# Optimization experiments

Hardware: AMD Instinct MI355X
Metric: run time of the kernel (lower is better)

## Reference

```python
import jax, jax.numpy as jnp
import numpy as np

B, N, DIM = 2, 2048, 2048
N_HEAD, N_KV_HEAD = 32, 8
HEAD_DIM = DIM // N_HEAD  # 64
NEG_INF = -1e9


def setup_inputs() -> dict:
    key = jax.random.key(0)
    ks = jax.random.split(key, 4)
    x = jax.random.normal(ks[0], (B, N, DIM), dtype=jnp.float32)
    Wq = jax.random.normal(ks[1], (DIM, N_HEAD * HEAD_DIM), dtype=jnp.float32) * (DIM ** -0.5)
    Wkv = jax.random.normal(ks[2], (DIM, 2 * N_KV_HEAD * HEAD_DIM), dtype=jnp.float32) * (DIM ** -0.5)
    Wo = jax.random.normal(ks[3], (N_HEAD * HEAD_DIM, DIM), dtype=jnp.float32) * (DIM ** -0.5)
    # RoPE angles: freqs = 1/theta^(2i/d), angle[p, i] = p * freqs[i]
    freqs = 1.0 / (10000.0 ** (jnp.arange(0, HEAD_DIM, 2, dtype=jnp.float32) / HEAD_DIM))
    angles = jnp.arange(N, dtype=jnp.float32)[:, None] * freqs[None, :]  # (N, HEAD_DIM//2)
    rope_cos = jnp.cos(angles)
    rope_sin = jnp.sin(angles)
    # additive causal mask (n, n)
    mask = jnp.where(jnp.tril(jnp.ones((N, N), dtype=bool)), 0.0, NEG_INF).astype(jnp.float32)
    return {"x": x, "Wq": Wq, "Wkv": Wkv, "Wo": Wo, "rope_cos": rope_cos, "rope_sin": rope_sin, "mask": mask, "start_pos": 0}


def apply_rope(x, cos, sin):
    # x: (b, n, h, d); cos/sin: (n, d//2). Complex mult on interleaved pairs.
    xr = x.reshape(*x.shape[:-1], HEAD_DIM // 2, 2)
    xe, xo = xr[..., 0], xr[..., 1]
    c = cos[None, :, None, :]
    s = sin[None, :, None, :]
    yr = xe * c - xo * s
    yi = xe * s + xo * c
    return jnp.stack([yr, yi], axis=-1).reshape(x.shape)


def reference(x, Wq, Wkv, Wo, rope_cos, rope_sin, mask, start_pos):
    b, n, _ = x.shape
    q = (x @ Wq).reshape(b, n, N_HEAD, HEAD_DIM)
    kv = (x @ Wkv).reshape(b, n, 2, N_KV_HEAD, HEAD_DIM)
    k, v = kv[:, :, 0], kv[:, :, 1]
    q = apply_rope(q, rope_cos, rope_sin)
    k = apply_rope(k, rope_cos, rope_sin)
    # repeat kv heads: 'b n h d -> b n (r h) d'
    r = N_HEAD // N_KV_HEAD
    k = jnp.tile(k, (1, 1, r, 1))
    v = jnp.tile(v, (1, 1, r, 1))
    scale = HEAD_DIM ** -0.5
    attn = jnp.einsum('bnhd,bmhd->bhnm', q, k) * scale + mask[None, None]
    attn = jax.nn.softmax(attn, axis=-1)
    out = jnp.einsum('bhnm,bmhd->bnhd', attn, v).reshape(b, n, N_HEAD * HEAD_DIM)
    return out @ Wo
```

## Files before the change

kernel.cpp:

```cpp
#include <hip/hip_runtime.h>


#define BSZ  2
#define NSEQ 2048
#define DIMD 2048
#define NH   32
#define NKV  8
#define HD   64
#define TK   32

typedef __bf16 bf16x8 __attribute__((ext_vector_type(8)));
typedef __bf16 bf16x4 __attribute__((ext_vector_type(4)));
typedef __bf16 bf16x2 __attribute__((ext_vector_type(2)));
typedef float  floatx4 __attribute__((ext_vector_type(4)));
typedef float  floatx16 __attribute__((ext_vector_type(16)));
typedef unsigned int uintx4 __attribute__((ext_vector_type(4)));

#define MFMA16(a, b, c) __builtin_amdgcn_mfma_f32_16x16x32_bf16(a, b, c, 0, 0, 0)
#define MFMA32(a, b, c) __builtin_amdgcn_mfma_f32_32x32x16_bf16(a, b, c, 0, 0, 0)

#define WAITV(n) asm volatile("s_waitcnt vmcnt(" #n ")" ::: "memory")

__device__ __forceinline__ void barrier_nodrain() {
    asm volatile("" ::: "memory");
    __builtin_amdgcn_sched_barrier(0);
    __builtin_amdgcn_s_barrier();
    __builtin_amdgcn_sched_barrier(0);
    asm volatile("" ::: "memory");
}

__device__ __forceinline__ void gload_lds16(const void* g, void* l) {
    __builtin_amdgcn_global_load_lds((const __attribute__((address_space(1))) void*)g,
                                     (__attribute__((address_space(3))) void*)l, 16, 0, 0);
}

__device__ __forceinline__ unsigned pk2(float a, float b) {
    bf16x2 t; t[0] = (__bf16)a; t[1] = (__bf16)b;
    return __builtin_bit_cast(unsigned, t);
}

__global__ void cvt_x_kernel(const float* __restrict__ in, __bf16* __restrict__ out, int n4) {
    int i = blockIdx.x * blockDim.x + threadIdx.x;
    if (i >= n4) return;
    float4 v = ((const float4*)in)[i];
    bf16x4 o;
    o[0] = (__bf16)v.x; o[1] = (__bf16)v.y; o[2] = (__bf16)v.z; o[3] = (__bf16)v.w;
    ((bf16x4*)out)[i] = o;
}

__global__ void transpose_cvt_kernel(const float* __restrict__ W, __bf16* __restrict__ Wt,
                                     int C, int K) {
    __shared__ float t[32][33];
    int c0 = blockIdx.x * 32, r0 = blockIdx.y * 32;
    int lx = threadIdx.x & 31, ly = threadIdx.x >> 5;
    for (int i = 0; i < 32; i += 8)
        t[ly + i][lx] = W[(size_t)(r0 + ly + i) * C + c0 + lx];
    __syncthreads();
    for (int i = 0; i < 32; i += 8)
        Wt[(size_t)(c0 + ly + i) * K + r0 + lx] = (__bf16)t[lx][ly + i];
}


#define MMAC(mh, nh)                                                           \
    {                                                                          \
        asm volatile("s_waitcnt lgkmcnt(0)" ::: "memory");                     \
        __builtin_amdgcn_sched_barrier(0);                                     \
        __builtin_amdgcn_s_setprio(1);                                         \
        _Pragma("unroll")                                                      \
        for (int il = 0; il < 4; ++il)                                         \
            _Pragma("unroll")                                                  \
            for (int jl = 0; jl < 2; ++jl)                                     \
                _Pragma("unroll")                                              \
                for (int ks = 0; ks < 2; ++ks)                                 \
                    acc[(mh) * 4 + il][(nh) * 2 + jl] =                        \
                        MFMA16(af[il][ks], bfr[jl][ks],                        \
                               acc[(mh) * 4 + il][(nh) * 2 + jl]);             \
        __builtin_amdgcn_s_setprio(0);                                         \
        barrier_nodrain();                                                     \
    }

__device__ __forceinline__ void gemm256_8ph(const __bf16* __restrict__ Ap,
                                            const __bf16* __restrict__ Bp,
                                            __bf16* As, __bf16* Bs,
                                            floatx4 (&acc)[8][4]) {
    int tid = threadIdx.x;
    int wave = tid >> 6, lane = tid & 63;
    int wm = wave >> 2, wn = wave & 3;
    int quad = lane >> 4, l16 = lane & 15;
    int swk = l16 & 7;

    int srcc = ((tid & 7) ^ ((tid >> 3) & 7)) << 3;
    int srow = tid >> 3;
    int wb = wave * 512;

    auto stage = [&](const __bf16* panel, __bf16* region, int kt) {
        gload_lds16(panel + (size_t)srow * DIMD + kt * 64 + srcc, region + wb);
        gload_lds16(panel + (size_t)(64 + srow) * DIMD + kt * 64 + srcc,
                    region + 4096 + wb);
    };

    bf16x8 af[4][2], bfr[2][2];
    auto rdA = [&](const __bf16* R) {
        #pragma unroll
        for (int il = 0; il < 4; ++il) {
            int rl = (2 * il + wm) * 16 + l16;
            #pragma unroll
            for (int ks = 0; ks < 2; ++ks)
                af[il][ks] = *(const bf16x8*)&R[rl * 64 + (((ks * 4 + quad) ^ swk) << 3)];
        }
    };
    auto rdB = [&](const __bf16* R) {
        #pragma unroll
        for (int jl = 0; jl < 2; ++jl) {
            int rl = (4 * jl + wn) * 16 + l16;
            #pragma unroll
            for (int ks = 0; ks < 2; ++ks)
                bfr[jl][ks] = *(const bf16x8*)&R[rl * 64 + (((ks * 4 + quad) ^ swk) << 3)];
        }
    };

    const __bf16* ApH1 = Ap + (size_t)128 * DIMD;
    const __bf16* BpH1 = Bp + (size_t)128 * DIMD;

    stage(Ap,   As + 0,    0);  stage(ApH1, As + 8192, 0);
    stage(Bp,   Bs + 0,    0);  stage(BpH1, Bs + 8192, 0);
    stage(Ap,   As + 16384, 1); stage(BpH1, Bs + 16384 + 8192, 1);

    #pragma unroll 2
    for (int t = 0; t < TK; ++t) {
        int b = t & 1;
        __bf16* Ab  = As + (b << 14);
        __bf16* Bb  = Bs + (b << 14);
        __bf16* Aob = As + ((b ^ 1) << 14);
        __bf16* Bob = Bs + ((b ^ 1) << 14);

        if (t < TK - 1) { WAITV(4); } else { WAITV(0); }
        barrier_nodrain();

        rdA(Ab);
        rdB(Bb);
        if (t + 1 < TK) stage(ApH1, Aob + 8192, t + 1);
        MMAC(0, 0);
        rdB(Bb + 8192);
        if (t + 1 < TK) stage(Bp, Bob, t + 1);
        MMAC(0, 1);
        rdA(Ab + 8192);
        if (t + 2 < TK) stage(Ap, Ab, t + 2);
        MMAC(1, 1);
        rdB(Bb);
        if (t + 2 < TK) stage(BpH1, Bb + 8192, t + 2);
        MMAC(1, 0);
    }
}

#define AROW(i) (((i) >> 2 << 7) + ((2 * ((i) & 3) + wm) << 4) + (quad << 2))
#define BCOL(j) (((j) >> 1 << 7) + ((4 * ((j) & 1) + wn) << 4) + l16)

__global__ __launch_bounds__(512, 2) void gemm_qkv_kernel(
    const __bf16* __restrict__ A, const __bf16* __restrict__ Bt,
    const float* __restrict__ cosb, const float* __restrict__ sinb,
    __bf16* __restrict__ Qo, __bf16* __restrict__ Ko, __bf16* __restrict__ Vo) {
    __shared__ __align__(16) __bf16 As[2 * 2 * 8192];
    __shared__ __align__(16) __bf16 Bs[2 * 2 * 8192];
    int p0 = blockIdx.x * 256;
    int t0 = blockIdx.y * 256;

    floatx4 acc[8][4] = {};
    gemm256_8ph(Bt + (size_t)p0 * DIMD, A + (size_t)t0 * DIMD, As, Bs, acc);

    int tid = threadIdx.x;
    int wave = tid >> 6, lane = tid & 63;
    int wm = wave >> 2, wn = wave & 3;
    int quad = lane >> 4, l16 = lane & 15;
    bool isQ = p0 < 2048;
    bool isV = p0 >= 2560;
    const float sc = isQ ? 0.18033688f : 1.0f;

    #pragma unroll
    for (int i = 0; i < 8; ++i) {
        int pp = p0 + AROW(i);
        int dq = pp & 63;
        #pragma unroll
        for (int j = 0; j < 4; ++j) {
            int t = t0 + BCOL(j);
            int b = t >> 11, n = t & 2047;
            float x0 = acc[i][j][0], x1 = acc[i][j][1];
            float x2 = acc[i][j][2], x3 = acc[i][j][3];
            if (!isV) {
                int d2 = dq >> 1;
                float2 cv = *(const float2*)(cosb + (size_t)n * 32 + d2);
                float2 sv = *(const float2*)(sinb + (size_t)n * 32 + d2);
                bf16x4 o;
                o[0] = (__bf16)((x0 * cv.x - x1 * sv.x) * sc);
                o[1] = (__bf16)((x0 * sv.x + x1 * cv.x) * sc);
                o[2] = (__bf16)((x2 * cv.y - x3 * sv.y) * sc);
                o[3] = (__bf16)((x2 * sv.y + x3 * cv.y) * sc);
                if (isQ) {
                    int h = pp >> 6;
                    *(bf16x4*)&Qo[((size_t)(b * NH + h) * NSEQ + n) * HD + dq] = o;
                } else {
                    int kvh = (pp - 2048) >> 6;
                    *(bf16x4*)&Ko[((size_t)(b * NKV + kvh) * NSEQ + n) * HD + dq] = o;
                }
            } else {
                int kvh = (pp - 2560) >> 6;
                size_t base = (size_t)(b * NKV + kvh) * HD;
                Vo[(base + dq + 0) * NSEQ + n] = (__bf16)x0;
                Vo[(base + dq + 1) * NSEQ + n] = (__bf16)x1;
                Vo[(base + dq + 2) * NSEQ + n] = (__bf16)x2;
                Vo[(base + dq + 3) * NSEQ + n] = (__bf16)x3;
            }
        }
    }
}

__global__ __launch_bounds__(512, 2) void gemm_out_kernel(
    const __bf16* __restrict__ A, const __bf16* __restrict__ Bt,
    float* __restrict__ C) {
    __shared__ __align__(16) __bf16 As[2 * 2 * 8192];
    __shared__ __align__(16) __bf16 Bs[2 * 2 * 8192];
    int n0 = blockIdx.x * 256;
    int m0 = blockIdx.y * 256;

    floatx4 acc[8][4] = {};
    gemm256_8ph(A + (size_t)m0 * DIMD, Bt + (size_t)n0 * DIMD, As, Bs, acc);

    int tid = threadIdx.x;
    int wave = tid >> 6, lane = tid & 63;
    int wm = wave >> 2, wn = wave & 3;
    int quad = lane >> 4, l16 = lane & 15;
    #pragma unroll
    for (int i = 0; i < 8; ++i) {
        int row = m0 + AROW(i);
        #pragma unroll
        for (int j = 0; j < 4; ++j) {
            int col = n0 + BCOL(j);
            float* Cp = C + (size_t)row * 2048 + col;
            Cp[0]    = acc[i][j][0];
            Cp[2048] = acc[i][j][1];
            Cp[4096] = acc[i][j][2];
            Cp[6144] = acc[i][j][3];
        }
    }
}

__global__ __launch_bounds__(512) void attn_kernel(
    const __bf16* __restrict__ Q, const __bf16* __restrict__ K,
    const __bf16* __restrict__ Vt, __bf16* __restrict__ O) {
    __shared__ __align__(16) __bf16 Kl[2][64 * 64];
    __shared__ __align__(16) __bf16 Vl[2][64 * 64];

    int tid = threadIdx.x;
    int wave = tid >> 6, lane = tid & 63;
    int l31 = lane & 31, hi = lane >> 5;
    int bk = blockIdx.x;
    int b = bk >> 3, kvh = bk & 7;
    int j = 31 - (int)blockIdx.y;
    int w01 = wave & 1;
    int h = kvh + 8 * (wave >> 1);
    int q0 = (2 * j + w01) * 32;

    const __bf16* Qbase = Q + ((size_t)(b * NH + h)) * NSEQ * HD;
    const __bf16* Kbase = K + ((size_t)(b * NKV + kvh)) * NSEQ * HD;
    const __bf16* Vbase = Vt + ((size_t)(b * NKV + kvh)) * HD * NSEQ;
    int swl = (l31 & 7) << 3;

    auto stage = [&](int kt, int bi) {
        int row = tid >> 3;
        int el = ((tid & 7) << 3) ^ ((row & 7) << 3);
        gload_lds16(Kbase + (size_t)kt * 4096 + row * 64 + el, &Kl[bi][wave * 512]);
        gload_lds16(Vbase + (size_t)row * NSEQ + kt * 64 + el, &Vl[bi][wave * 512]);
    };

    bf16x8 qf[4];
    #pragma unroll
    for (int t = 0; t < 4; ++t)
        qf[t] = *(const bf16x8*)(Qbase + (size_t)(q0 + l31) * HD + t * 16 + hi * 8);

    floatx16 oacc[2] = {};
    float lsum = 0.0f;
    int pb = 0;
    stage(0, 0);

    for (int kt = 0; kt <= j; ++kt) {
        __syncthreads();
        if (kt < j) stage(kt + 1, pb ^ 1);
        const __bf16* Kp = &Kl[pb][0];
        const __bf16* Vp = &Vl[pb][0];
        bool diag = (kt == j);

        #pragma unroll
        for (int kvt = 0; kvt < 2; ++kvt) {
            if (diag && !w01 && kvt == 1) continue;
            bool domask = diag && (kvt == w01);

            floatx16 s = {};
            #pragma unroll
            for (int t = 0; t < 4; ++t) {
                bf16x8 ka = *(const bf16x8*)&Kp[(kvt * 32 + l31) * 64 +
                                                ((t * 16 + hi * 8) ^ swl)];
                s = MFMA32(ka, qf[t], s);
            }

            #pragma unroll
            for (int ks = 0; ks < 2; ++ks) {
                float e[8];
                if (domask) {
                    int q_l = q0 + l31;
                    #pragma unroll
                    for (int r = 0; r < 8; ++r) {
                        int kv = kt * 64 + kvt * 32 + ks * 16 +
                                 (r & 3) + 8 * (r >> 2) + 4 * hi;
                        float p = __builtin_exp2f(s[ks * 8 + r]);
                        e[r] = (kv > q_l) ? 0.0f : p;
                    }
                } else {
                    #pragma unroll
                    for (int r = 0; r < 8; ++r)
                        e[r] = __builtin_exp2f(s[ks * 8 + r]);
                }
                #pragma unroll
                for (int r = 0; r < 8; ++r) lsum += e[r];

                unsigned a0 = pk2(e[0], e[1]), a1 = pk2(e[2], e[3]);
                unsigned b0 = pk2(e[4], e[5]), b1 = pk2(e[6], e[7]);
                unsigned t0 = hi ? a0 : b0, t1 = hi ? a1 : b1;
                unsigned s0 = (unsigned)__shfl_xor((int)t0, 32, 64);
                unsigned s1 = (unsigned)__shfl_xor((int)t1, 32, 64);
                uintx4 fw;
                fw[0] = hi ? s0 : a0;
                fw[1] = hi ? s1 : a1;
                fw[2] = hi ? b0 : s0;
                fw[3] = hi ? b1 : s1;
                bf16x8 pfrag = __builtin_bit_cast(bf16x8, fw);

                #pragma unroll
                for (int dt = 0; dt < 2; ++dt) {
                    bf16x8 va = *(const bf16x8*)&Vp[(dt * 32 + l31) * 64 +
                                    ((kvt * 32 + ks * 16 + hi * 8) ^ swl)];
                    oacc[dt] = MFMA32(va, pfrag, oacc[dt]);
                }
            }
        }
        pb ^= 1;
    }

    lsum += __shfl_xor(lsum, 32, 64);
    float inv = 1.0f / lsum;
    __bf16* Op = O + ((size_t)(b * NSEQ + q0 + l31)) * (NH * HD) + h * HD;
    #pragma unroll
    for (int dt = 0; dt < 2; ++dt)
        #pragma unroll
        for (int g = 0; g < 4; ++g) {
            bf16x4 ov;
            #pragma unroll
            for (int r = 0; r < 4; ++r) ov[r] = (__bf16)(oacc[dt][4 * g + r] * inv);
            *(bf16x4*)(Op + dt * 32 + 8 * g + 4 * hi) = ov;
        }
}

extern "C" void kernel_launch(void* const* d_in, const int* in_sizes, int n_in,
                              void* d_out, int out_size, void* d_ws, size_t ws_size,
                              hipStream_t stream) {
    const float* x   = (const float*)d_in[0];
    const float* Wq  = (const float*)d_in[1];
    const float* Wkv = (const float*)d_in[2];
    const float* Wo  = (const float*)d_in[3];
    const float* rc  = (const float*)d_in[4];
    const float* rs  = (const float*)d_in[5];
    float* out = (float*)d_out;
    char* ws = (char*)d_ws;

    __bf16* xb    = (__bf16*)(ws + 0);
    __bf16* wqkvt = (__bf16*)(ws + 16777216);
    __bf16* wot   = (__bf16*)(ws + 29360128);
    __bf16* Qb    = (__bf16*)(ws + 37748736);
    __bf16* Kb    = (__bf16*)(ws + 54525952);
    __bf16* Vtb   = (__bf16*)(ws + 58720256);
    __bf16* attnb = (__bf16*)(ws + 62914560);

    cvt_x_kernel<<<8192, 256, 0, stream>>>(x, xb, 2097152);
    transpose_cvt_kernel<<<dim3(64, 64), 256, 0, stream>>>(Wq, wqkvt, 2048, 2048);
    transpose_cvt_kernel<<<dim3(32, 64), 256, 0, stream>>>(Wkv, wqkvt + (size_t)2048 * 2048, 1024, 2048);
    transpose_cvt_kernel<<<dim3(64, 64), 256, 0, stream>>>(Wo, wot, 2048, 2048);

    gemm_qkv_kernel<<<dim3(12, 16), 512, 0, stream>>>(xb, wqkvt, rc, rs, Qb, Kb, Vtb);

    attn_kernel<<<dim3(16, 32), 512, 0, stream>>>(Qb, Kb, Vtb, attnb);

    gemm_out_kernel<<<dim3(8, 16), 512, 0, stream>>>(attnb, wot, out);
}
```

Before: 340.3 us.

## Balance causal attention with paired query tiles and shrink output GEMM tile

```diff
diff --git a/kernel.cpp b/kernel.cpp
--- a/kernel.cpp
+++ b/kernel.cpp
@@ -155,6 +155,104 @@
 
 #define AROW(i) (((i) >> 2 << 7) + ((2 * ((i) & 3) + wm) << 4) + (quad << 2))
 #define BCOL(j) (((j) >> 1 << 7) + ((4 * ((j) & 1) + wn) << 4) + l16)
+
+
+#define MMAC_O(mh, nh)                                                         \
+    {                                                                          \
+        asm volatile("s_waitcnt lgkmcnt(0)" ::: "memory");                     \
+        __builtin_amdgcn_sched_barrier(0);                                     \
+        __builtin_amdgcn_s_setprio(1);                                         \
+        _Pragma("unroll")                                                      \
+        for (int il = 0; il < 2; ++il)                                         \
+            _Pragma("unroll")                                                  \
+            for (int jl = 0; jl < 2; ++jl)                                     \
+                _Pragma("unroll")                                              \
+                for (int ks = 0; ks < 2; ++ks)                                 \
+                    acc[(mh) * 2 + il][(nh) * 2 + jl] =                        \
+                        MFMA16(af[il][ks], bfr[jl][ks],                        \
+                               acc[(mh) * 2 + il][(nh) * 2 + jl]);             \
+        __builtin_amdgcn_s_setprio(0);                                         \
+        barrier_nodrain();                                                     \
+    }
+
+__device__ __forceinline__ void gemm128x256_8ph(const __bf16* __restrict__ Ap,
+                                                const __bf16* __restrict__ Bp,
+                                                __bf16* As, __bf16* Bs,
+                                                floatx4 (&acc)[4][4]) {
+    int tid = threadIdx.x;
+    int wave = tid >> 6, lane = tid & 63;
+    int wm = wave >> 2, wn = wave & 3;
+    int quad = lane >> 4, l16 = lane & 15;
+    int swk = l16 & 7;
+
+    int srcc = ((tid & 7) ^ ((tid >> 3) & 7)) << 3;
+    int srow = tid >> 3;
+    int wb = wave * 512;
+
+    auto stageA = [&](const __bf16* panel, __bf16* region, int kt) {
+        gload_lds16(panel + (size_t)srow * DIMD + kt * 64 + srcc, region + wb);
+    };
+    auto stageB = [&](const __bf16* panel, __bf16* region, int kt) {
+        gload_lds16(panel + (size_t)srow * DIMD + kt * 64 + srcc, region + wb);
+        gload_lds16(panel + (size_t)(64 + srow) * DIMD + kt * 64 + srcc,
+                    region + 4096 + wb);
+    };
+
+    bf16x8 af[2][2], bfr[2][2];
+    auto rdA = [&](const __bf16* R) {
+        #pragma unroll
+        for (int il = 0; il < 2; ++il) {
+            int rl = (2 * il + wm) * 16 + l16;
+            #pragma unroll
+            for (int ks = 0; ks < 2; ++ks)
+                af[il][ks] = *(const bf16x8*)&R[rl * 64 + (((ks * 4 + quad) ^ swk) << 3)];
+        }
+    };
+    auto rdB = [&](const __bf16* R) {
+        #pragma unroll
+        for (int jl = 0; jl < 2; ++jl) {
+            int rl = (4 * jl + wn) * 16 + l16;
+            #pragma unroll
+            for (int ks = 0; ks < 2; ++ks)
+                bfr[jl][ks] = *(const bf16x8*)&R[rl * 64 + (((ks * 4 + quad) ^ swk) << 3)];
+        }
+    };
+
+    const __bf16* ApH1 = Ap + (size_t)64 * DIMD;
+    const __bf16* BpH1 = Bp + (size_t)128 * DIMD;
+
+    stageA(Ap,   As + 0,    0);  stageA(ApH1, As + 4096, 0);
+    stageB(Bp,   Bs + 0,    0);  stageB(BpH1, Bs + 8192, 0);
+    stageA(Ap,   As + 8192, 1);  stageB(BpH1, Bs + 16384 + 8192, 1);
+
+    #pragma unroll 2
+    for (int t = 0; t < TK; ++t) {
+        int b = t & 1;
+        __bf16* Ab  = As + (b << 13);
+        __bf16* Bb  = Bs + (b << 14);
+        __bf16* Aob = As + ((b ^ 1) << 13);
+        __bf16* Bob = Bs + ((b ^ 1) << 14);
+
+        if (t < TK - 1) { WAITV(3); } else { WAITV(0); }
+        barrier_nodrain();
+
+        rdA(Ab);
+        rdB(Bb);
+        if (t + 1 < TK) stageA(ApH1, Aob + 4096, t + 1);
+        MMAC_O(0, 0);
+        rdB(Bb + 8192);
+        if (t + 1 < TK) stageB(Bp, Bob, t + 1);
+        MMAC_O(0, 1);
+        rdA(Ab + 4096);
+        if (t + 2 < TK) stageA(Ap, Ab, t + 2);
+        MMAC_O(1, 1);
+        rdB(Bb);
+        if (t + 2 < TK) stageB(BpH1, Bb + 8192, t + 2);
+        MMAC_O(1, 0);
+    }
+}
+
+#define AROW128(i) (((i) >> 1) * 64 + ((2 * ((i) & 1) + wm) << 4) + (quad << 2))
 
 __global__ __launch_bounds__(512, 2) void gemm_qkv_kernel(
     const __bf16* __restrict__ A, const __bf16* __restrict__ Bt,
@@ -217,21 +315,21 @@
 __global__ __launch_bounds__(512, 2) void gemm_out_kernel(
     const __bf16* __restrict__ A, const __bf16* __restrict__ Bt,
     float* __restrict__ C) {
-    __shared__ __align__(16) __bf16 As[2 * 2 * 8192];
+    __shared__ __align__(16) __bf16 As[2 * 8192];
     __shared__ __align__(16) __bf16 Bs[2 * 2 * 8192];
     int n0 = blockIdx.x * 256;
-    int m0 = blockIdx.y * 256;
-
-    floatx4 acc[8][4] = {};
-    gemm256_8ph(A + (size_t)m0 * DIMD, Bt + (size_t)n0 * DIMD, As, Bs, acc);
+    int m0 = blockIdx.y * 128;
+
+    floatx4 acc[4][4] = {};
+    gemm128x256_8ph(A + (size_t)m0 * DIMD, Bt + (size_t)n0 * DIMD, As, Bs, acc);
 
     int tid = threadIdx.x;
     int wave = tid >> 6, lane = tid & 63;
     int wm = wave >> 2, wn = wave & 3;
     int quad = lane >> 4, l16 = lane & 15;
     #pragma unroll
-    for (int i = 0; i < 8; ++i) {
-        int row = m0 + AROW(i);
+    for (int i = 0; i < 4; ++i) {
+        int row = m0 + AROW128(i);
         #pragma unroll
         for (int j = 0; j < 4; ++j) {
             int col = n0 + BCOL(j);
@@ -244,7 +342,7 @@
     }
 }
 
-__global__ __launch_bounds__(512) void attn_kernel(
+__global__ __launch_bounds__(256) void attn_kernel(
     const __bf16* __restrict__ Q, const __bf16* __restrict__ K,
     const __bf16* __restrict__ Vt, __bf16* __restrict__ O) {
     __shared__ __align__(16) __bf16 Kl[2][64 * 64];
@@ -255,10 +353,8 @@
     int l31 = lane & 31, hi = lane >> 5;
     int bk = blockIdx.x;
     int b = bk >> 3, kvh = bk & 7;
-    int j = 31 - (int)blockIdx.y;
-    int w01 = wave & 1;
-    int h = kvh + 8 * (wave >> 1);
-    int q0 = (2 * j + w01) * 32;
+    int h = kvh + 8 * wave;
+    int y = blockIdx.y;
 
     const __bf16* Qbase = Q + ((size_t)(b * NH + h)) * NSEQ * HD;
     const __bf16* Kbase = K + ((size_t)(b * NKV + kvh)) * NSEQ * HD;
@@ -266,97 +362,111 @@
     int swl = (l31 & 7) << 3;
 
     auto stage = [&](int kt, int bi) {
-        int row = tid >> 3;
-        int el = ((tid & 7) << 3) ^ ((row & 7) << 3);
-        gload_lds16(Kbase + (size_t)kt * 4096 + row * 64 + el, &Kl[bi][wave * 512]);
-        gload_lds16(Vbase + (size_t)row * NSEQ + kt * 64 + el, &Vl[bi][wave * 512]);
-    };
-
-    bf16x8 qf[4];
-    #pragma unroll
-    for (int t = 0; t < 4; ++t)
-        qf[t] = *(const bf16x8*)(Qbase + (size_t)(q0 + l31) * HD + t * 16 + hi * 8);
-
-    floatx16 oacc[2] = {};
-    float lsum = 0.0f;
+        #pragma unroll
+        for (int r = 0; r < 2; ++r) {
+            int obase = r * 2048 + wave * 512;
+            int o = obase + lane * 8;
+            int row = o >> 6;
+            int el = (o & 63) ^ ((row & 7) << 3);
+            gload_lds16(Kbase + (size_t)kt * 4096 + row * 64 + el, &Kl[bi][obase]);
+            gload_lds16(Vbase + (size_t)row * NSEQ + kt * 64 + el, &Vl[bi][obase]);
+        }
+    };
+
     int pb = 0;
     stage(0, 0);
 
-    for (int kt = 0; kt <= j; ++kt) {
-        __syncthreads();
-        if (kt < j) stage(kt + 1, pb ^ 1);
-        const __bf16* Kp = &Kl[pb][0];
-        const __bf16* Vp = &Vl[pb][0];
-        bool diag = (kt == j);
-
-        #pragma unroll
-        for (int kvt = 0; kvt < 2; ++kvt) {
-            if (diag && !w01 && kvt == 1) continue;
-            bool domask = diag && (kvt == w01);
-
-            floatx16 s = {};
+    for (int ph = 0; ph < 2; ++ph) {
+        int qt = ph ? y : 63 - y;
+        int q0 = qt * 32;
+        int J = (q0 + 31) >> 6;
+        int par = qt & 1;
+
+        bf16x8 qf[4];
+        #pragma unroll
+        for (int t = 0; t < 4; ++t)
+            qf[t] = *(const bf16x8*)(Qbase + (size_t)(q0 + l31) * HD + t * 16 + hi * 8);
+
+        floatx16 oacc[2] = {};
+        float lsum = 0.0f;
+
+        for (int kt = 0; kt <= J; ++kt) {
+            __syncthreads();
+            if (kt < J) stage(kt + 1, pb ^ 1);
+            else if (ph == 0) stage(0, pb ^ 1);
+            const __bf16* Kp = &Kl[pb][0];
+            const __bf16* Vp = &Vl[pb][0];
+            bool diag = (kt == J);
+
             #pragma unroll
-            for (int t = 0; t < 4; ++t) {
-                bf16x8 ka = *(const bf16x8*)&Kp[(kvt * 32 + l31) * 64 +
-                                                ((t * 16 + hi * 8) ^ swl)];
-                s = MFMA32(ka, qf[t], s);
-            }
-
-            #pragma unroll
-            for (int ks = 0; ks < 2; ++ks) {
-                float e[8];
-                if (domask) {
-                    int q_l = q0 + l31;
+            for (int kvt = 0; kvt < 2; ++kvt) {
+                if (diag && !par && kvt == 1) continue;
+                bool domask = diag && (kvt == par);
+
+                floatx16 s = {};
+                #pragma unroll
+                for (int t = 0; t < 4; ++t) {
+                    bf16x8 ka = *(const bf16x8*)&Kp[(kvt * 32 + l31) * 64 +
+                                                    ((t * 16 + hi * 8) ^ swl)];
+                    s = MFMA32(ka, qf[t], s);
+                }
+
+                #pragma unroll
+                for (int ks = 0; ks < 2; ++ks) {
+                    float e[8];
+                    if (domask) {
+                        int q_l = q0 + l31;
+                        #pragma unroll
+                        for (int r = 0; r < 8; ++r) {
+                            int kv = kt * 64 + kvt * 32 + ks * 16 +
+                                     (r & 3) + 8 * (r >> 2) + 4 * hi;
+                            float p = __builtin_exp2f(s[ks * 8 + r]);
+                            e[r] = (kv > q_l) ? 0.0f : p;
+                        }
+                    } else {
+                        #pragma unroll
+                        for (int r = 0; r < 8; ++r)
+                            e[r] = __builtin_exp2f(s[ks * 8 + r]);
+                    }
                     #pragma unroll
-                    for (int r = 0; r < 8; ++r) {
-                        int kv = kt * 64 + kvt * 32 + ks * 16 +
-                                 (r & 3) + 8 * (r >> 2) + 4 * hi;
-                        float p = __builtin_exp2f(s[ks * 8 + r]);
-                        e[r] = (kv > q_l) ? 0.0f : p;
+                    for (int r = 0; r < 8; ++r) lsum += e[r];
+
+                    unsigned a0 = pk2(e[0], e[1]), a1 = pk2(e[2], e[3]);
+                    unsigned b0 = pk2(e[4], e[5]), b1 = pk2(e[6], e[7]);
+                    unsigned t0 = hi ? a0 : b0, t1 = hi ? a1 : b1;
+                    unsigned s0 = (unsigned)__shfl_xor((int)t0, 32, 64);
+                    unsigned s1 = (unsigned)__shfl_xor((int)t1, 32, 64);
+                    uintx4 fw;
+                    fw[0] = hi ? s0 : a0;
+                    fw[1] = hi ? s1 : a1;
+                    fw[2] = hi ? b0 : s0;
+                    fw[3] = hi ? b1 : s1;
+                    bf16x8 pfrag = __builtin_bit_cast(bf16x8, fw);
+
+                    #pragma unroll
+                    for (int dt = 0; dt < 2; ++dt) {
+                        bf16x8 va = *(const bf16x8*)&Vp[(dt * 32 + l31) * 64 +
+                                        ((kvt * 32 + ks * 16 + hi * 8) ^ swl)];
+                        oacc[dt] = MFMA32(va, pfrag, oacc[dt]);
                     }
-                } else {
-                    #pragma unroll
-                    for (int r = 0; r < 8; ++r)
-                        e[r] = __builtin_exp2f(s[ks * 8 + r]);
-                }
-                #pragma unroll
-                for (int r = 0; r < 8; ++r) lsum += e[r];
-
-                unsigned a0 = pk2(e[0], e[1]), a1 = pk2(e[2], e[3]);
-                unsigned b0 = pk2(e[4], e[5]), b1 = pk2(e[6], e[7]);
-                unsigned t0 = hi ? a0 : b0, t1 = hi ? a1 : b1;
-                unsigned s0 = (unsigned)__shfl_xor((int)t0, 32, 64);
-                unsigned s1 = (unsigned)__shfl_xor((int)t1, 32, 64);
-                uintx4 fw;
-                fw[0] = hi ? s0 : a0;
-                fw[1] = hi ? s1 : a1;
-                fw[2] = hi ? b0 : s0;
-                fw[3] = hi ? b1 : s1;
-                bf16x8 pfrag = __builtin_bit_cast(bf16x8, fw);
-
-                #pragma unroll
-                for (int dt = 0; dt < 2; ++dt) {
-                    bf16x8 va = *(const bf16x8*)&Vp[(dt * 32 + l31) * 64 +
-                                    ((kvt * 32 + ks * 16 + hi * 8) ^ swl)];
-                    oacc[dt] = MFMA32(va, pfrag, oacc[dt]);
                 }
             }
-        }
-        pb ^= 1;
-    }
-
-    lsum += __shfl_xor(lsum, 32, 64);
-    float inv = 1.0f / lsum;
-    __bf16* Op = O + ((size_t)(b * NSEQ + q0 + l31)) * (NH * HD) + h * HD;
-    #pragma unroll
-    for (int dt = 0; dt < 2; ++dt)
-        #pragma unroll
-        for (int g = 0; g < 4; ++g) {
-            bf16x4 ov;
+            pb ^= 1;
+        }
+
+        lsum += __shfl_xor(lsum, 32, 64);
+        float inv = 1.0f / lsum;
+        __bf16* Op = O + ((size_t)(b * NSEQ + q0 + l31)) * (NH * HD) + h * HD;
+        #pragma unroll
+        for (int dt = 0; dt < 2; ++dt)
             #pragma unroll
-            for (int r = 0; r < 4; ++r) ov[r] = (__bf16)(oacc[dt][4 * g + r] * inv);
-            *(bf16x4*)(Op + dt * 32 + 8 * g + 4 * hi) = ov;
-        }
+            for (int g = 0; g < 4; ++g) {
+                bf16x4 ov;
+                #pragma unroll
+                for (int r = 0; r < 4; ++r) ov[r] = (__bf16)(oacc[dt][4 * g + r] * inv);
+                *(bf16x4*)(Op + dt * 32 + 8 * g + 4 * hi) = ov;
+            }
+    }
 }
 
 extern "C" void kernel_launch(void* const* d_in, const int* in_sizes, int n_in,
@@ -386,7 +496,7 @@
 
     gemm_qkv_kernel<<<dim3(12, 16), 512, 0, stream>>>(xb, wqkvt, rc, rs, Qb, Kb, Vtb);
 
-    attn_kernel<<<dim3(16, 32), 512, 0, stream>>>(Qb, Kb, Vtb, attnb);
-
-    gemm_out_kernel<<<dim3(8, 16), 512, 0, stream>>>(attnb, wot, out);
-}
+    attn_kernel<<<dim3(16, 32), 256, 0, stream>>>(Qb, Kb, Vtb, attnb);
+
+    gemm_out_kernel<<<dim3(8, 32), 512, 0, stream>>>(attnb, wot, out);
+}
```

Result: faster. 322.7 us (-5.2%).
